# Optimization experiments

Hardware: AMD Instinct MI355X
Metric: run time of the kernel (lower is better)

Reference implementation:

```python
import jax, jax.numpy as jnp
import numpy as np

L, D, H, FF = 6, 768, 12, 3072
DH = D // H
EPS = 1e-12

def _layer_norm(x, g, b):
    mu = jnp.mean(x, axis=-1, keepdims=True)
    var = jnp.mean((x - mu) ** 2, axis=-1, keepdims=True)
    return (x - mu) * jax.lax.rsqrt(var + EPS) * g + b

def setup_inputs() -> dict:
    key = jax.random.key(0)
    ks = jax.random.split(key, 12)
    s = 0.02
    inp = {
        "x": jax.random.normal(ks[0], (8, 512, D), dtype=jnp.float32),
        "attn_mask": jnp.ones((8, 512), dtype=jnp.int32),
        "Wq": jax.random.normal(ks[1], (L, D, D), dtype=jnp.float32) * s,
        "bq": jnp.zeros((L, D), dtype=jnp.float32),
        "Wk": jax.random.normal(ks[2], (L, D, D), dtype=jnp.float32) * s,
        "bk": jnp.zeros((L, D), dtype=jnp.float32),
        "Wv": jax.random.normal(ks[3], (L, D, D), dtype=jnp.float32) * s,
        "bv": jnp.zeros((L, D), dtype=jnp.float32),
        "Wo": jax.random.normal(ks[4], (L, D, D), dtype=jnp.float32) * s,
        "bo": jnp.zeros((L, D), dtype=jnp.float32),
        "ln1_g": jnp.ones((L, D), dtype=jnp.float32),
        "ln1_b": jnp.zeros((L, D), dtype=jnp.float32),
        "W1": jax.random.normal(ks[5], (L, D, FF), dtype=jnp.float32) * s,
        "b1": jnp.zeros((L, FF), dtype=jnp.float32),
        "W2": jax.random.normal(ks[6], (L, FF, D), dtype=jnp.float32) * s,
        "b2": jnp.zeros((L, D), dtype=jnp.float32),
        "ln2_g": jnp.ones((L, D), dtype=jnp.float32),
        "ln2_b": jnp.zeros((L, D), dtype=jnp.float32),
    }
    return inp

def reference(x, attn_mask, Wq, bq, Wk, bk, Wv, bv, Wo, bo,
              ln1_g, ln1_b, W1, b1, W2, b2, ln2_g, ln2_b):
    bs, S, _ = x.shape
    mask_neg = (attn_mask == 0)[:, None, None, :]  # (bs,1,1,S)
    h = x
    for i in range(L):
        def split_heads(t):
            return t.reshape(bs, S, H, DH).transpose(0, 2, 1, 3)  # (bs,H,S,dh)
        q = split_heads(h @ Wq[i] + bq[i]) / jnp.sqrt(jnp.float32(DH))
        k = split_heads(h @ Wk[i] + bk[i])
        v = split_heads(h @ Wv[i] + bv[i])
        scores = jnp.einsum('bhqd,bhkd->bhqk', q, k)
        scores = jnp.where(mask_neg, jnp.float32(-1e9), scores)
        w = jax.nn.softmax(scores, axis=-1)
        ctx = jnp.einsum('bhqk,bhkd->bhqd', w, v)
        ctx = ctx.transpose(0, 2, 1, 3).reshape(bs, S, D)
        sa = ctx @ Wo[i] + bo[i]
        h2 = _layer_norm(sa + h, ln1_g[i], ln1_b[i])
        ffn = jax.nn.gelu(h2 @ W1[i] + b1[i], approximate=False) @ W2[i] + b2[i]
        h = _layer_norm(ffn + h2, ln2_g[i], ln2_b[i])
    return h
```

## Files before the change

kernel.cpp:

```cpp
#include <hip/hip_runtime.h>
#include <math.h>

#define NLAYER 6
#define DMODEL 768
#define NHEAD 12
#define DHEAD 64
#define FFDIM 3072
#define SEQ 512
#define BATCH 8
#define NTOK (BATCH * SEQ)
#define ND ((size_t)NTOK * DMODEL)

typedef __bf16 bf16_t;
typedef __bf16 bf16x8 __attribute__((ext_vector_type(8)));
typedef float f32x4 __attribute__((ext_vector_type(4)));

__device__ __forceinline__ float bf2f(ushort u) {
    return __uint_as_float(((unsigned int)u) << 16);
}
union BFU { __bf16 h; ushort u; };
__device__ __forceinline__ ushort f2b(float x) { BFU c; c.h = (__bf16)x; return c.u; }

#define GLDS(gp, lp) __builtin_amdgcn_global_load_lds( \
    (const __attribute__((address_space(1))) void*)(gp), \
    (__attribute__((address_space(3))) void*)(lp), 16, 0, 0)

__global__ __launch_bounds__(256) void gemm_mfma(
    const ushort* __restrict__ A, const ushort* __restrict__ Bt,
    const float* __restrict__ bias, float* __restrict__ Cf,
    ushort* __restrict__ Cb, int M, int K, int N, int act)
{
    __shared__ __align__(16) ushort As[4096];
    __shared__ __align__(16) ushort Bs[4096];

    const int t = threadIdx.x;
    const int w = t >> 6, l = t & 63;
    const int wr = w >> 1, wc = w & 1;
    const int row0 = blockIdx.y * 128, col0 = blockIdx.x * 128;

    f32x4 acc[4][4];
#pragma unroll
    for (int mi = 0; mi < 4; ++mi)
#pragma unroll
        for (int ni = 0; ni < 4; ++ni)
#pragma unroll
            for (int e = 0; e < 4; ++e) acc[mi][ni][e] = 0.f;

    const int c0 = t,       r0 = c0 >> 2, kg0 = (c0 & 3) ^ ((r0 >> 1) & 3);
    const int c1 = t + 256, r1 = c1 >> 2, kg1 = (c1 & 3) ^ ((r1 >> 1) & 3);
    const ushort* gA0 = A + (size_t)(row0 + r0) * K + kg0 * 8;
    const ushort* gA1 = A + (size_t)(row0 + r1) * K + kg1 * 8;
    const ushort* gB0 = Bt + (size_t)(col0 + r0) * K + kg0 * 8;
    const ushort* gB1 = Bt + (size_t)(col0 + r1) * K + kg1 * 8;
    ushort* lA0 = &As[w * 512];
    ushort* lA1 = &As[2048 + w * 512];
    ushort* lB0 = &Bs[w * 512];
    ushort* lB1 = &Bs[2048 + w * 512];

    const int lm = l & 15, lq = l >> 4;
    int aoff[4], boff[4];
#pragma unroll
    for (int mi = 0; mi < 4; ++mi) {
        int m = wr * 64 + mi * 16 + lm;
        aoff[mi] = m * 32 + (lq ^ ((m >> 1) & 3)) * 8;
    }
#pragma unroll
    for (int ni = 0; ni < 4; ++ni) {
        int n = wc * 64 + ni * 16 + lm;
        boff[ni] = n * 32 + (lq ^ ((n >> 1) & 3)) * 8;
    }

    for (int k0 = 0; k0 < K; k0 += 32) {
        GLDS(gA0 + k0, lA0);
        GLDS(gA1 + k0, lA1);
        GLDS(gB0 + k0, lB0);
        GLDS(gB1 + k0, lB1);
        __syncthreads();

        bf16x8 af[4], bfr[4];
#pragma unroll
        for (int mi = 0; mi < 4; ++mi) af[mi] = *(const bf16x8*)&As[aoff[mi]];
#pragma unroll
        for (int ni = 0; ni < 4; ++ni) bfr[ni] = *(const bf16x8*)&Bs[boff[ni]];

#pragma unroll
        for (int mi = 0; mi < 4; ++mi)
#pragma unroll
            for (int ni = 0; ni < 4; ++ni)
                acc[mi][ni] = __builtin_amdgcn_mfma_f32_16x16x32_bf16(
                    af[mi], bfr[ni], acc[mi][ni], 0, 0, 0);
        __syncthreads();
    }

#pragma unroll
    for (int mi = 0; mi < 4; ++mi) {
        int rowb = row0 + wr * 64 + mi * 16 + lq * 4;
#pragma unroll
        for (int ni = 0; ni < 4; ++ni) {
            int col = col0 + wc * 64 + ni * 16 + lm;
            float bv = bias[col];
#pragma unroll
            for (int r = 0; r < 4; ++r) {
                float v = acc[mi][ni][r] + bv;
                if (act == 1) v = 0.5f * v * (1.0f + erff(v * 0.70710678118654752f));
                size_t idx = (size_t)(rowb + r) * N + col;
                if (Cb) ((bf16_t*)Cb)[idx] = (bf16_t)v;
                else    Cf[idx] = v;
            }
        }
    }
}

__global__ __launch_bounds__(256) void gemm_qkv(
    const ushort* __restrict__ A, const ushort* __restrict__ Bt,
    const float* __restrict__ bq, const float* __restrict__ bk,
    const float* __restrict__ bv,
    ushort* __restrict__ qb, ushort* __restrict__ kb, ushort* __restrict__ vtb)
{
    __shared__ __align__(16) ushort As[4096];
    __shared__ __align__(16) ushort Bs[4096];

    const int K = DMODEL;
    const int t = threadIdx.x;
    const int w = t >> 6, l = t & 63;
    const int wr = w >> 1, wc = w & 1;
    const int row0 = blockIdx.y * 128, col0 = blockIdx.x * 128;
    const int seg = blockIdx.x / 6;

    f32x4 acc[4][4];
#pragma unroll
    for (int mi = 0; mi < 4; ++mi)
#pragma unroll
        for (int ni = 0; ni < 4; ++ni)
#pragma unroll
            for (int e = 0; e < 4; ++e) acc[mi][ni][e] = 0.f;

    const int c0 = t,       r0 = c0 >> 2, kg0 = (c0 & 3) ^ ((r0 >> 1) & 3);
    const int c1 = t + 256, r1 = c1 >> 2, kg1 = (c1 & 3) ^ ((r1 >> 1) & 3);
    const ushort* gA0 = A + (size_t)(row0 + r0) * K + kg0 * 8;
    const ushort* gA1 = A + (size_t)(row0 + r1) * K + kg1 * 8;
    const ushort* gB0 = Bt + (size_t)(col0 + r0) * K + kg0 * 8;
    const ushort* gB1 = Bt + (size_t)(col0 + r1) * K + kg1 * 8;
    ushort* lA0 = &As[w * 512];
    ushort* lA1 = &As[2048 + w * 512];
    ushort* lB0 = &Bs[w * 512];
    ushort* lB1 = &Bs[2048 + w * 512];

    const int lm = l & 15, lq = l >> 4;
    int aoff[4], boff[4];
#pragma unroll
    for (int mi = 0; mi < 4; ++mi) {
        int m = wr * 64 + mi * 16 + lm;
        aoff[mi] = m * 32 + (lq ^ ((m >> 1) & 3)) * 8;
    }
#pragma unroll
    for (int ni = 0; ni < 4; ++ni) {
        int n = wc * 64 + ni * 16 + lm;
        boff[ni] = n * 32 + (lq ^ ((n >> 1) & 3)) * 8;
    }

    for (int k0 = 0; k0 < K; k0 += 32) {
        GLDS(gA0 + k0, lA0);
        GLDS(gA1 + k0, lA1);
        GLDS(gB0 + k0, lB0);
        GLDS(gB1 + k0, lB1);
        __syncthreads();

        bf16x8 af[4], bfr[4];
#pragma unroll
        for (int mi = 0; mi < 4; ++mi) af[mi] = *(const bf16x8*)&As[aoff[mi]];
#pragma unroll
        for (int ni = 0; ni < 4; ++ni) bfr[ni] = *(const bf16x8*)&Bs[boff[ni]];

#pragma unroll
        for (int mi = 0; mi < 4; ++mi)
#pragma unroll
            for (int ni = 0; ni < 4; ++ni)
                acc[mi][ni] = __builtin_amdgcn_mfma_f32_16x16x32_bf16(
                    af[mi], bfr[ni], acc[mi][ni], 0, 0, 0);
        __syncthreads();
    }

    const float* bp = (seg == 0) ? bq : (seg == 1) ? bk : bv;
    const float sc = (seg == 0) ? 0.125f : 1.0f;
#pragma unroll
    for (int mi = 0; mi < 4; ++mi) {
        int rowb = row0 + wr * 64 + mi * 16 + lq * 4;
#pragma unroll
        for (int ni = 0; ni < 4; ++ni) {
            int col = col0 + wc * 64 + ni * 16 + lm;
            int lcol = col - seg * 768;
            float bvv = bp[lcol];
            if (seg == 2) {
                int hh = lcol >> 6, dd = lcol & 63;
                int bb = rowb >> 9, ss = rowb & 511;
                ushort4 o;
                o.x = f2b(acc[mi][ni][0] + bvv);
                o.y = f2b(acc[mi][ni][1] + bvv);
                o.z = f2b(acc[mi][ni][2] + bvv);
                o.w = f2b(acc[mi][ni][3] + bvv);
                *(ushort4*)&vtb[(((size_t)(bb * NHEAD + hh)) * DHEAD + dd) * SEQ + ss] = o;
            } else {
                ushort* dst = seg ? kb : qb;
#pragma unroll
                for (int r = 0; r < 4; ++r)
                    dst[(size_t)(rowb + r) * DMODEL + lcol] = f2b((acc[mi][ni][r] + bvv) * sc);
            }
        }
    }
}

#define QSTR 72

__global__ __launch_bounds__(256) void attn_mfma(
    const ushort* __restrict__ qb, const ushort* __restrict__ kb,
    const ushort* __restrict__ vtb, const int* __restrict__ mask,
    ushort* __restrict__ ctxb)
{
    __shared__ __align__(16) ushort Qs[64 * QSTR];
    __shared__ __align__(16) ushort Ks[64 * QSTR];
    __shared__ __align__(16) ushort Vs[64 * QSTR];
    __shared__ __align__(16) ushort Ps[64 * QSTR];
    __shared__ float Ma[64];

    const int qt = blockIdx.x, h = blockIdx.y, b = blockIdx.z;
    const int t = threadIdx.x;
    const int w = t >> 6, l = t & 63;
    const int lm = l & 15, lq = l >> 4;

#pragma unroll
    for (int i = 0; i < 2; ++i) {
        int ch = t + i * 256;
        int r = ch >> 3, c8 = ch & 7;
        *(uint4*)&Qs[r * QSTR + c8 * 8] =
            *(const uint4*)&qb[((size_t)(b * SEQ + qt * 64 + r)) * DMODEL + h * DHEAD + c8 * 8];
    }

    f32x4 O[4];
#pragma unroll
    for (int n0 = 0; n0 < 4; ++n0)
#pragma unroll
        for (int e = 0; e < 4; ++e) O[n0][e] = 0.f;
    float mrow[4] = {-3.4e38f, -3.4e38f, -3.4e38f, -3.4e38f};
    float lrow[4] = {0.f, 0.f, 0.f, 0.f};

    const int qrow = w * 16 + lm;
    const int prow = w * 16 + lq * 4;

    for (int kt = 0; kt < SEQ / 64; ++kt) {
#pragma unroll
        for (int i = 0; i < 2; ++i) {
            int ch = t + i * 256;
            int r = ch >> 3, c8 = ch & 7;
            *(uint4*)&Ks[r * QSTR + c8 * 8] =
                *(const uint4*)&kb[((size_t)(b * SEQ + kt * 64 + r)) * DMODEL + h * DHEAD + c8 * 8];
            *(uint4*)&Vs[r * QSTR + c8 * 8] =
                *(const uint4*)&vtb[(((size_t)(b * NHEAD + h)) * DHEAD + r) * SEQ + kt * 64 + c8 * 8];
        }
        if (t < 64) Ma[t] = (mask[b * SEQ + kt * 64 + t] == 0) ? -1e9f : 0.f;
        __syncthreads();

        bf16x8 aq0 = *(const bf16x8*)&Qs[qrow * QSTR + lq * 8];
        bf16x8 aq1 = *(const bf16x8*)&Qs[qrow * QSTR + lq * 8 + 32];
        f32x4 S[4];
#pragma unroll
        for (int n0 = 0; n0 < 4; ++n0) {
#pragma unroll
            for (int e = 0; e < 4; ++e) S[n0][e] = 0.f;
            bf16x8 b0 = *(const bf16x8*)&Ks[(n0 * 16 + lm) * QSTR + lq * 8];
            bf16x8 b1 = *(const bf16x8*)&Ks[(n0 * 16 + lm) * QSTR + lq * 8 + 32];
            S[n0] = __builtin_amdgcn_mfma_f32_16x16x32_bf16(aq0, b0, S[n0], 0, 0, 0);
            S[n0] = __builtin_amdgcn_mfma_f32_16x16x32_bf16(aq1, b1, S[n0], 0, 0, 0);
        }

        float ma4[4];
#pragma unroll
        for (int n0 = 0; n0 < 4; ++n0) ma4[n0] = Ma[n0 * 16 + lm];
#pragma unroll
        for (int n0 = 0; n0 < 4; ++n0)
#pragma unroll
            for (int r = 0; r < 4; ++r) S[n0][r] += ma4[n0];

        float tm[4];
#pragma unroll
        for (int r = 0; r < 4; ++r)
            tm[r] = fmaxf(fmaxf(S[0][r], S[1][r]), fmaxf(S[2][r], S[3][r]));
#pragma unroll
        for (int off = 1; off < 16; off <<= 1)
#pragma unroll
            for (int r = 0; r < 4; ++r)
                tm[r] = fmaxf(tm[r], __shfl_xor(tm[r], off, 64));

        float al[4], ts[4];
#pragma unroll
        for (int r = 0; r < 4; ++r) {
            float mn = fmaxf(mrow[r], tm[r]);
            al[r] = __expf(mrow[r] - mn);
            mrow[r] = mn;
            ts[r] = 0.f;
        }
#pragma unroll
        for (int n0 = 0; n0 < 4; ++n0)
#pragma unroll
            for (int r = 0; r < 4; ++r) {
                float p = __expf(S[n0][r] - mrow[r]);
                ts[r] += p;
                Ps[(prow + r) * QSTR + n0 * 16 + lm] = f2b(p);
            }
#pragma unroll
        for (int off = 1; off < 16; off <<= 1)
#pragma unroll
            for (int r = 0; r < 4; ++r)
                ts[r] += __shfl_xor(ts[r], off, 64);
#pragma unroll
        for (int r = 0; r < 4; ++r) lrow[r] = lrow[r] * al[r] + ts[r];
#pragma unroll
        for (int n0 = 0; n0 < 4; ++n0)
#pragma unroll
            for (int r = 0; r < 4; ++r) O[n0][r] *= al[r];

        bf16x8 ap0 = *(const bf16x8*)&Ps[qrow * QSTR + lq * 8];
        bf16x8 ap1 = *(const bf16x8*)&Ps[qrow * QSTR + lq * 8 + 32];
#pragma unroll
        for (int n0 = 0; n0 < 4; ++n0) {
            bf16x8 v0 = *(const bf16x8*)&Vs[(n0 * 16 + lm) * QSTR + lq * 8];
            bf16x8 v1 = *(const bf16x8*)&Vs[(n0 * 16 + lm) * QSTR + lq * 8 + 32];
            O[n0] = __builtin_amdgcn_mfma_f32_16x16x32_bf16(ap0, v0, O[n0], 0, 0, 0);
            O[n0] = __builtin_amdgcn_mfma_f32_16x16x32_bf16(ap1, v1, O[n0], 0, 0, 0);
        }
        __syncthreads();
    }

    float inv[4];
#pragma unroll
    for (int r = 0; r < 4; ++r) inv[r] = 1.f / lrow[r];
#pragma unroll
    for (int n0 = 0; n0 < 4; ++n0)
#pragma unroll
        for (int r = 0; r < 4; ++r)
            Ks[(prow + r) * QSTR + n0 * 16 + lm] = f2b(O[n0][r] * inv[r]);
    __syncthreads();
#pragma unroll
    for (int i = 0; i < 2; ++i) {
        int ch = t + i * 256;
        int r = ch >> 3, c8 = ch & 7;
        *(uint4*)&ctxb[((size_t)(b * SEQ + qt * 64 + r)) * DMODEL + h * DHEAD + c8 * 8] =
            *(const uint4*)&Ks[r * QSTR + c8 * 8];
    }
}

__global__ __launch_bounds__(256) void transpose_w(
    const float* __restrict__ Wq, const float* __restrict__ Wk,
    const float* __restrict__ Wv, const float* __restrict__ Wo,
    const float* __restrict__ W1, const float* __restrict__ W2,
    ushort* __restrict__ Wqt, ushort* __restrict__ Wkt,
    ushort* __restrict__ Wvt, ushort* __restrict__ Wot,
    ushort* __restrict__ W1t, ushort* __restrict__ W2t)
{
    __shared__ float tile[32][33];
    const int bid = blockIdx.x;
    const float* src; ushort* dst; int K, N, tx, ty;
    if (bid < 2304) {
        int m = bid / 576, tl = bid % 576;
        src = (m == 0) ? Wq : (m == 1) ? Wk : (m == 2) ? Wv : Wo;
        dst = (m == 0) ? Wqt : (m == 1) ? Wkt : (m == 2) ? Wvt : Wot;
        K = 768; N = 768; tx = tl % 24; ty = tl / 24;
    } else if (bid < 4608) {
        int tl = bid - 2304;
        src = W1; dst = W1t; K = 768; N = 3072; tx = tl % 96; ty = tl / 96;
    } else {
        int tl = bid - 4608;
        src = W2; dst = W2t; K = 3072; N = 768; tx = tl % 24; ty = tl / 24;
    }
    const int t = threadIdx.x;
    const int lx = t & 31, ly = t >> 5;
    const int n0 = tx * 32, k0 = ty * 32;
#pragma unroll
    for (int i = 0; i < 4; ++i)
        tile[lx][ly + i * 8] = src[(size_t)(k0 + ly + i * 8) * N + n0 + lx];
    __syncthreads();
#pragma unroll
    for (int i = 0; i < 4; ++i)
        ((bf16_t*)dst)[(size_t)(n0 + ly + i * 8) * K + k0 + lx] =
            (bf16_t)tile[ly + i * 8][lx];
}

__global__ __launch_bounds__(256) void f2bf_kernel(
    const float* __restrict__ src, ushort* __restrict__ dst)
{
    const size_t i = ((size_t)blockIdx.x * 256 + threadIdx.x) * 4;
    float4 v = *(const float4*)(src + i);
    ushort4 o;
    o.x = f2b(v.x); o.y = f2b(v.y); o.z = f2b(v.z); o.w = f2b(v.w);
    *(ushort4*)(dst + i) = o;
}

__global__ __launch_bounds__(256) void add_ln_kernel(
    const float* __restrict__ a, const float* __restrict__ b,
    const float* __restrict__ gw, const float* __restrict__ bw,
    float* __restrict__ out, ushort* __restrict__ outb)
{
    const int row = blockIdx.x;
    const int t = threadIdx.x;
    __shared__ float red[8];

    const float* ar = a + (size_t)row * DMODEL;
    const float* br = b + (size_t)row * DMODEL;

    float vals[3];
    float s = 0.f;
#pragma unroll
    for (int i = 0; i < 3; ++i) {
        vals[i] = ar[t + i * 256] + br[t + i * 256];
        s += vals[i];
    }
#pragma unroll
    for (int off = 32; off > 0; off >>= 1) s += __shfl_down(s, off, 64);
    if ((t & 63) == 0) red[t >> 6] = s;
    __syncthreads();
    const float mu = (red[0] + red[1] + red[2] + red[3]) * (1.0f / DMODEL);

    float vs = 0.f;
#pragma unroll
    for (int i = 0; i < 3; ++i) {
        float d = vals[i] - mu;
        vs += d * d;
    }
#pragma unroll
    for (int off = 32; off > 0; off >>= 1) vs += __shfl_down(vs, off, 64);
    if ((t & 63) == 0) red[4 + (t >> 6)] = vs;
    __syncthreads();
    const float var = (red[4] + red[5] + red[6] + red[7]) * (1.0f / DMODEL);
    const float inv = rsqrtf(var + 1e-12f);

#pragma unroll
    for (int i = 0; i < 3; ++i) {
        int c = t + i * 256;
        float v = (vals[i] - mu) * inv * gw[c] + bw[c];
        out[(size_t)row * DMODEL + c] = v;
        ((bf16_t*)outb)[(size_t)row * DMODEL + c] = (bf16_t)v;
    }
}

extern "C" void kernel_launch(void* const* d_in, const int* in_sizes, int n_in,
                              void* d_out, int out_size, void* d_ws, size_t ws_size,
                              hipStream_t stream)
{
    const float* x    = (const float*)d_in[0];
    const int*   mask = (const int*)d_in[1];
    const float* Wq = (const float*)d_in[2];
    const float* bq = (const float*)d_in[3];
    const float* Wk = (const float*)d_in[4];
    const float* bk = (const float*)d_in[5];
    const float* Wv = (const float*)d_in[6];
    const float* bv = (const float*)d_in[7];
    const float* Wo = (const float*)d_in[8];
    const float* bo = (const float*)d_in[9];
    const float* ln1g = (const float*)d_in[10];
    const float* ln1b = (const float*)d_in[11];
    const float* W1 = (const float*)d_in[12];
    const float* b1 = (const float*)d_in[13];
    const float* W2 = (const float*)d_in[14];
    const float* b2 = (const float*)d_in[15];
    const float* ln2g = (const float*)d_in[16];
    const float* ln2b = (const float*)d_in[17];

    float* f32b = (float*)d_ws;
    float* hbuf = f32b;
    float* f1   = f32b + ND;
    float* h2   = f32b + 2 * ND;
    ushort* ub  = (ushort*)(f32b + 3 * ND);
    ushort* qb  = ub;
    ushort* kb  = ub + ND;
    ushort* vtb = ub + 2 * ND;
    ushort* hb  = ub + 3 * ND;
    ushort* U   = ub + 4 * ND;
    ushort* ctxb = U;
    ushort* Wqkvt = U + (size_t)NTOK * FFDIM;
    ushort* Wot = Wqkvt + 3 * 768 * 768;
    ushort* W1t = Wot + 768 * 768;
    ushort* W2t = W1t + (size_t)768 * 3072;

    hipMemcpyAsync(hbuf, x, ND * sizeof(float), hipMemcpyDeviceToDevice, stream);
    f2bf_kernel<<<(int)(ND / 1024), 256, 0, stream>>>(x, hb);

    const dim3 gQKV(18, 32);
    const dim3 gD(6, 32);
    const dim3 gFF(24, 32);
    const dim3 gA(SEQ / 64, NHEAD, BATCH);

    for (int l = 0; l < NLAYER; ++l) {
        const float* Wq_l = Wq + (size_t)l * DMODEL * DMODEL;
        const float* Wk_l = Wk + (size_t)l * DMODEL * DMODEL;
        const float* Wv_l = Wv + (size_t)l * DMODEL * DMODEL;
        const float* Wo_l = Wo + (size_t)l * DMODEL * DMODEL;
        const float* W1_l = W1 + (size_t)l * DMODEL * FFDIM;
        const float* W2_l = W2 + (size_t)l * FFDIM * DMODEL;

        transpose_w<<<6912, 256, 0, stream>>>(Wq_l, Wk_l, Wv_l, Wo_l, W1_l, W2_l,
                                              Wqkvt, Wqkvt + 768 * 768,
                                              Wqkvt + 2 * 768 * 768, Wot, W1t, W2t);

        gemm_qkv<<<gQKV, 256, 0, stream>>>(hb, Wqkvt,
                                           bq + (size_t)l * DMODEL,
                                           bk + (size_t)l * DMODEL,
                                           bv + (size_t)l * DMODEL,
                                           qb, kb, vtb);

        attn_mfma<<<gA, 256, 0, stream>>>(qb, kb, vtb, mask, ctxb);

        gemm_mfma<<<gD, 256, 0, stream>>>(ctxb, Wot, bo + (size_t)l * DMODEL,
                                          f1, nullptr, NTOK, DMODEL, DMODEL, 0);

        add_ln_kernel<<<NTOK, 256, 0, stream>>>(f1, hbuf, ln1g + (size_t)l * DMODEL,
                                                ln1b + (size_t)l * DMODEL, h2, hb);

        gemm_mfma<<<gFF, 256, 0, stream>>>(hb, W1t, b1 + (size_t)l * FFDIM,
                                           nullptr, U, NTOK, DMODEL, FFDIM, 1);
        gemm_mfma<<<gD, 256, 0, stream>>>(U, W2t, b2 + (size_t)l * DMODEL,
                                          f1, nullptr, NTOK, FFDIM, DMODEL, 0);

        float* hout = (l == NLAYER - 1) ? (float*)d_out : hbuf;
        add_ln_kernel<<<NTOK, 256, 0, stream>>>(f1, h2, ln2g + (size_t)l * DMODEL,
                                                ln2b + (size_t)l * DMODEL, hout, hb);
    }
}
```

Baseline: 1.487 ms.

## Split-K the N=768 GEMMs in two and reduce partials in layernorm

The output-projection and FFN-down GEMMs, which had only 192 blocks, now run as a two-way split-K grid of 384 blocks. Each half writes fp32 partial sums, with bias added only by the first. The add+layernorm kernel now sums both partials plus the residual, so no separate reduction kernel is needed. This aims to fill more compute units at the cost of writing and reading an extra fp32 activation-sized buffer, stored in the q/k bf16 workspace that is dead at that point.

```diff
diff --git a/kernel.cpp b/kernel.cpp
--- a/kernel.cpp
+++ b/kernel.cpp
@@ -107,6 +107,90 @@
                 if (Cb) ((bf16_t*)Cb)[idx] = (bf16_t)v;
                 else    Cf[idx] = v;
             }
+        }
+    }
+}
+
+__global__ __launch_bounds__(256) void gemm_mfma_sk(
+    const ushort* __restrict__ A, const ushort* __restrict__ Bt,
+    const float* __restrict__ bias, float* __restrict__ P0,
+    float* __restrict__ P1, int M, int K, int N, int kLen)
+{
+    __shared__ __align__(16) ushort As[4096];
+    __shared__ __align__(16) ushort Bs[4096];
+
+    const int t = threadIdx.x;
+    const int w = t >> 6, l = t & 63;
+    const int wr = w >> 1, wc = w & 1;
+    const int row0 = blockIdx.y * 128, col0 = blockIdx.x * 128;
+    const int z = blockIdx.z;
+    const int kOff = z * kLen;
+    float* Pz = (z == 0) ? P0 : P1;
+
+    f32x4 acc[4][4];
+#pragma unroll
+    for (int mi = 0; mi < 4; ++mi)
+#pragma unroll
+        for (int ni = 0; ni < 4; ++ni)
+#pragma unroll
+            for (int e = 0; e < 4; ++e) acc[mi][ni][e] = 0.f;
+
+    const int c0 = t,       r0 = c0 >> 2, kg0 = (c0 & 3) ^ ((r0 >> 1) & 3);
+    const int c1 = t + 256, r1 = c1 >> 2, kg1 = (c1 & 3) ^ ((r1 >> 1) & 3);
+    const ushort* gA0 = A + (size_t)(row0 + r0) * K + kg0 * 8;
+    const ushort* gA1 = A + (size_t)(row0 + r1) * K + kg1 * 8;
+    const ushort* gB0 = Bt + (size_t)(col0 + r0) * K + kg0 * 8;
+    const ushort* gB1 = Bt + (size_t)(col0 + r1) * K + kg1 * 8;
+    ushort* lA0 = &As[w * 512];
+    ushort* lA1 = &As[2048 + w * 512];
+    ushort* lB0 = &Bs[w * 512];
+    ushort* lB1 = &Bs[2048 + w * 512];
+
+    const int lm = l & 15, lq = l >> 4;
+    int aoff[4], boff[4];
+#pragma unroll
+    for (int mi = 0; mi < 4; ++mi) {
+        int m = wr * 64 + mi * 16 + lm;
+        aoff[mi] = m * 32 + (lq ^ ((m >> 1) & 3)) * 8;
+    }
+#pragma unroll
+    for (int ni = 0; ni < 4; ++ni) {
+        int n = wc * 64 + ni * 16 + lm;
+        boff[ni] = n * 32 + (lq ^ ((n >> 1) & 3)) * 8;
+    }
+
+    for (int k0 = kOff; k0 < kOff + kLen; k0 += 32) {
+        GLDS(gA0 + k0, lA0);
+        GLDS(gA1 + k0, lA1);
+        GLDS(gB0 + k0, lB0);
+        GLDS(gB1 + k0, lB1);
+        __syncthreads();
+
+        bf16x8 af[4], bfr[4];
+#pragma unroll
+        for (int mi = 0; mi < 4; ++mi) af[mi] = *(const bf16x8*)&As[aoff[mi]];
+#pragma unroll
+        for (int ni = 0; ni < 4; ++ni) bfr[ni] = *(const bf16x8*)&Bs[boff[ni]];
+
+#pragma unroll
+        for (int mi = 0; mi < 4; ++mi)
+#pragma unroll
+            for (int ni = 0; ni < 4; ++ni)
+                acc[mi][ni] = __builtin_amdgcn_mfma_f32_16x16x32_bf16(
+                    af[mi], bfr[ni], acc[mi][ni], 0, 0, 0);
+        __syncthreads();
+    }
+
+#pragma unroll
+    for (int mi = 0; mi < 4; ++mi) {
+        int rowb = row0 + wr * 64 + mi * 16 + lq * 4;
+#pragma unroll
+        for (int ni = 0; ni < 4; ++ni) {
+            int col = col0 + wc * 64 + ni * 16 + lm;
+            float bv = (z == 0) ? bias[col] : 0.f;
+#pragma unroll
+            for (int r = 0; r < 4; ++r)
+                Pz[(size_t)(rowb + r) * N + col] = acc[mi][ni][r] + bv;
         }
     }
 }
@@ -395,8 +479,9 @@
     *(ushort4*)(dst + i) = o;
 }
 
-__global__ __launch_bounds__(256) void add_ln_kernel(
-    const float* __restrict__ a, const float* __restrict__ b,
+__global__ __launch_bounds__(256) void add_ln3_kernel(
+    const float* __restrict__ p0, const float* __restrict__ p1,
+    const float* __restrict__ res,
     const float* __restrict__ gw, const float* __restrict__ bw,
     float* __restrict__ out, ushort* __restrict__ outb)
 {
@@ -404,14 +489,16 @@
     const int t = threadIdx.x;
     __shared__ float red[8];
 
-    const float* ar = a + (size_t)row * DMODEL;
-    const float* br = b + (size_t)row * DMODEL;
+    const float* a0 = p0 + (size_t)row * DMODEL;
+    const float* a1 = p1 + (size_t)row * DMODEL;
+    const float* rr = res + (size_t)row * DMODEL;
 
     float vals[3];
     float s = 0.f;
 #pragma unroll
     for (int i = 0; i < 3; ++i) {
-        vals[i] = ar[t + i * 256] + br[t + i * 256];
+        int c = t + i * 256;
+        vals[i] = a0[c] + a1[c] + rr[c];
         s += vals[i];
     }
 #pragma unroll
@@ -481,11 +568,13 @@
     ushort* W1t = Wot + 768 * 768;
     ushort* W2t = W1t + (size_t)768 * 3072;
 
+    float* p1 = (float*)ub;
+
     hipMemcpyAsync(hbuf, x, ND * sizeof(float), hipMemcpyDeviceToDevice, stream);
     f2bf_kernel<<<(int)(ND / 1024), 256, 0, stream>>>(x, hb);
 
     const dim3 gQKV(18, 32);
-    const dim3 gD(6, 32);
+    const dim3 gSK(6, 32, 2);
     const dim3 gFF(24, 32);
     const dim3 gA(SEQ / 64, NHEAD, BATCH);
 
@@ -509,19 +598,22 @@
 
         attn_mfma<<<gA, 256, 0, stream>>>(qb, kb, vtb, mask, ctxb);
 
-        gemm_mfma<<<gD, 256, 0, stream>>>(ctxb, Wot, bo + (size_t)l * DMODEL,
-                                          f1, nullptr, NTOK, DMODEL, DMODEL, 0);
-
-        add_ln_kernel<<<NTOK, 256, 0, stream>>>(f1, hbuf, ln1g + (size_t)l * DMODEL,
-                                                ln1b + (size_t)l * DMODEL, h2, hb);
+        gemm_mfma_sk<<<gSK, 256, 0, stream>>>(ctxb, Wot, bo + (size_t)l * DMODEL,
+                                              f1, p1, NTOK, DMODEL, DMODEL, DMODEL / 2);
+
+        add_ln3_kernel<<<NTOK, 256, 0, stream>>>(f1, p1, hbuf,
+                                                 ln1g + (size_t)l * DMODEL,
+                                                 ln1b + (size_t)l * DMODEL, h2, hb);
 
         gemm_mfma<<<gFF, 256, 0, stream>>>(hb, W1t, b1 + (size_t)l * FFDIM,
                                            nullptr, U, NTOK, DMODEL, FFDIM, 1);
-        gemm_mfma<<<gD, 256, 0, stream>>>(U, W2t, b2 + (size_t)l * DMODEL,
-                                          f1, nullptr, NTOK, FFDIM, DMODEL, 0);
+
+        gemm_mfma_sk<<<gSK, 256, 0, stream>>>(U, W2t, b2 + (size_t)l * DMODEL,
+                                              f1, p1, NTOK, FFDIM, DMODEL, FFDIM / 2);
 
         float* hout = (l == NLAYER - 1) ? (float*)d_out : hbuf;
-        add_ln_kernel<<<NTOK, 256, 0, stream>>>(f1, h2, ln2g + (size_t)l * DMODEL,
-                                                ln2b + (size_t)l * DMODEL, hout, hb);
-    }
-}
+        add_ln3_kernel<<<NTOK, 256, 0, stream>>>(f1, p1, h2,
+                                                 ln2g + (size_t)l * DMODEL,
+                                                 ln2b + (size_t)l * DMODEL, hout, hb);
+    }
+}
```

New measurement: 1.311 ms. -11.8%, faster.
